# Kernel tuning notes

Measured on AMD Instinct MI355X. Metric: run time of the kernel, lower is better.

## Reference

```python
import jax, jax.numpy as jnp
import numpy as np

B, S, D = 8, 4096, 512
H, DH = 8, 64  # heads, dim_head; inner_dim = H*DH = 512
EPS = 1e-6


def setup_inputs() -> dict:
    key = jax.random.key(0)
    ks = jax.random.split(key, 9)
    scale = 1.0 / np.sqrt(D)
    inner = H * DH
    return {
        "x": jax.random.normal(ks[0], (B, S, D), dtype=jnp.float32),
        "Wq": jax.random.normal(ks[1], (D, inner), dtype=jnp.float32) * scale,
        "bq": jax.random.normal(ks[2], (inner,), dtype=jnp.float32) * 0.01,
        "Wk": jax.random.normal(ks[3], (D, inner), dtype=jnp.float32) * scale,
        "bk": jax.random.normal(ks[4], (inner,), dtype=jnp.float32) * 0.01,
        "Wv": jax.random.normal(ks[5], (D, inner), dtype=jnp.float32) * scale,
        "bv": jax.random.normal(ks[6], (inner,), dtype=jnp.float32) * 0.01,
        "Wo": jax.random.normal(ks[7], (inner, D), dtype=jnp.float32) * (1.0 / np.sqrt(inner)),
        "bo": jax.random.normal(ks[8], (D,), dtype=jnp.float32) * 0.01,
    }


def _phi(x):
    # elu(x) + 1, the fast-transformers default feature map
    return jax.nn.elu(x) + 1.0


def reference(x, Wq, bq, Wk, bk, Wv, bv, Wo, bo):
    b, s, _ = x.shape
    q = (x @ Wq + bq).reshape(b, s, H, DH)
    k = (x @ Wk + bk).reshape(b, s, H, DH)
    v = (x @ Wv + bv).reshape(b, s, H, DH)

    Qf = _phi(q)  # [b, s, h, d]
    Kf = _phi(k)  # [b, s, h, d]

    # KV = sum_s Kf_s (outer) v_s  -> [b, h, d, m]
    KV = jnp.einsum('bshd,bshm->bhdm', Kf, v)
    # normalizer: Z = 1 / (Qf . sum_s Kf + eps)  -> [b, s, h]
    Ksum = Kf.sum(axis=1)  # [b, h, d]
    Z = 1.0 / (jnp.einsum('bshd,bhd->bsh', Qf, Ksum) + EPS)
    out = jnp.einsum('bshd,bhdm,bsh->bshm', Qf, KV, Z)  # [b, s, h, m]

    out = out.reshape(b, s, H * DH)
    return out @ Wo + bo  # dropout is identity at inference
```

## Files before the change

kernel.cpp:

```cpp
#include <hip/hip_runtime.h>
#include <hip/hip_fp16.h>


constexpr int Ss = 4096;
constexpr int Dd = 512;
constexpr int Hh = 8;
constexpr int Mtot = 8 * 4096;
constexpr float EPSF = 1e-6f;

typedef short v8s __attribute__((ext_vector_type(8)));
typedef float v4f __attribute__((ext_vector_type(4)));

__device__ __forceinline__ short f2bf(float f) {
  unsigned u = __float_as_uint(f);
  u += 0x7fff + ((u >> 16) & 1);
  return (short)(u >> 16);
}
__device__ __forceinline__ float bf2f(short s) {
  return __uint_as_float(((unsigned)(unsigned short)s) << 16);
}
__device__ __forceinline__ void async_cp16(const void* g, void* l) {
  __builtin_amdgcn_global_load_lds((__attribute__((address_space(1))) void*)g,
                                   (__attribute__((address_space(3))) void*)l, 16, 0, 0);
}

__global__ __launch_bounds__(256) void prep_w(
    const float* __restrict__ W0, const float* __restrict__ W1,
    const float* __restrict__ W2, const float* __restrict__ W3,
    short* __restrict__ Th, short* __restrict__ Tl)
{
  const float* W = (blockIdx.z == 0) ? W0 : (blockIdx.z == 1) ? W1
                  : (blockIdx.z == 2) ? W2 : W3;
  short* th = Th + (size_t)blockIdx.z * 512 * 512;
  short* tl = Tl + (size_t)blockIdx.z * 512 * 512;
  __shared__ float tile[32][33];
  const int t = threadIdx.x;
  const int tx = t & 31, ty = t >> 5;
  const int k0 = blockIdx.x * 32, n0 = blockIdx.y * 32;
#pragma unroll
  for (int r = 0; r < 32; r += 8)
    tile[ty + r][tx] = W[(size_t)(k0 + ty + r) * 512 + n0 + tx];
  __syncthreads();
#pragma unroll
  for (int r = 0; r < 32; r += 8) {
    const float v = tile[tx][ty + r];
    const short h = f2bf(v);
    const short l = f2bf(v - bf2f(h));
    th[(size_t)(n0 + ty + r) * 512 + k0 + tx] = h;
    tl[(size_t)(n0 + ty + r) * 512 + k0 + tx] = l;
  }
}

__global__ __launch_bounds__(256) void split_x(
    const float* __restrict__ X, short* __restrict__ H, short* __restrict__ L, int n4)
{
  const int i = blockIdx.x * 256 + threadIdx.x;
  if (i >= n4) return;
  const float4 x = reinterpret_cast<const float4*>(X)[i];
  short4 h, l;
  h.x = f2bf(x.x); l.x = f2bf(x.x - bf2f(h.x));
  h.y = f2bf(x.y); l.y = f2bf(x.y - bf2f(h.y));
  h.z = f2bf(x.z); l.z = f2bf(x.z - bf2f(h.z));
  h.w = f2bf(x.w); l.w = f2bf(x.w - bf2f(h.w));
  reinterpret_cast<short4*>(H)[i] = h;
  reinterpret_cast<short4*>(L)[i] = l;
}

__global__ __launch_bounds__(256) void gemm_qkv(
    const short* __restrict__ Ah, const short* __restrict__ Al,
    const short* __restrict__ Wth, const short* __restrict__ Wtl,
    const float* __restrict__ bq, const float* __restrict__ bk,
    const float* __restrict__ bv,
    __half* __restrict__ Qf, __half* __restrict__ Kf, __half* __restrict__ Vv)
{
  constexpr int K = 512;
  __shared__ short As_h[128 * 32], As_l[128 * 32], Bs_h[128 * 32], Bs_l[128 * 32];

  const int mat = blockIdx.y >> 2;
  const int col0 = (blockIdx.y & 3) * 128;
  const int row0 = blockIdx.x * 128;
  const short* Bh = Wth + (size_t)mat * K * 512;
  const short* Bl = Wtl + (size_t)mat * K * 512;
  const float* bias = (mat == 0) ? bq : (mat == 1) ? bk : bv;
  __half* Co = (mat == 0) ? Qf : (mat == 1) ? Kf : Vv;
  const int act = (mat < 2);

  const int t = threadIdx.x;
  const int lane = t & 63;
  const int wv = t >> 6;
  const int wm = wv & 1, wn = wv >> 1;
  const int mr = lane & 15, kq = lane >> 4;

  v4f acc[4][4];
#pragma unroll
  for (int i = 0; i < 4; ++i)
#pragma unroll
    for (int j = 0; j < 4; ++j) acc[i][j] = (v4f){0.f, 0.f, 0.f, 0.f};

  const int srow = t >> 2;
  const int spq = t & 3;

  for (int k0 = 0; k0 < K; k0 += 32) {
#pragma unroll
    for (int c = 0; c < 2; ++c) {
      const int m = c * 64 + srow;
      const int q = spq ^ ((m >> 1) & 3);
      const size_t ga = (size_t)(row0 + m) * K + k0 + q * 8;
      const size_t gb = (size_t)(col0 + m) * K + k0 + q * 8;
      const int lo = c * 2048 + wv * 512;
      async_cp16(Ah + ga, As_h + lo);
      async_cp16(Al + ga, As_l + lo);
      async_cp16(Bh + gb, Bs_h + lo);
      async_cp16(Bl + gb, Bs_l + lo);
    }
    __syncthreads();

    v8s fah[4], fal[4], fbh[4], fbl[4];
#pragma unroll
    for (int i = 0; i < 4; ++i) {
      const int ma = wm * 64 + i * 16 + mr;
      const int pa = kq ^ ((ma >> 1) & 3);
      fah[i] = *reinterpret_cast<const v8s*>(&As_h[ma * 32 + pa * 8]);
      fal[i] = *reinterpret_cast<const v8s*>(&As_l[ma * 32 + pa * 8]);
      const int nb = wn * 64 + i * 16 + mr;
      const int pb = kq ^ ((nb >> 1) & 3);
      fbh[i] = *reinterpret_cast<const v8s*>(&Bs_h[nb * 32 + pb * 8]);
      fbl[i] = *reinterpret_cast<const v8s*>(&Bs_l[nb * 32 + pb * 8]);
    }
#pragma unroll
    for (int i = 0; i < 4; ++i)
#pragma unroll
      for (int j = 0; j < 4; ++j) {
        acc[i][j] = __builtin_amdgcn_mfma_f32_16x16x32_bf16(fah[i], fbh[j], acc[i][j], 0, 0, 0);
        acc[i][j] = __builtin_amdgcn_mfma_f32_16x16x32_bf16(fah[i], fbl[j], acc[i][j], 0, 0, 0);
        acc[i][j] = __builtin_amdgcn_mfma_f32_16x16x32_bf16(fal[i], fbh[j], acc[i][j], 0, 0, 0);
      }
    __syncthreads();
  }

#pragma unroll
  for (int j = 0; j < 4; ++j) {
    const int nc = col0 + wn * 64 + j * 16 + mr;
    const float bz = bias[nc];
#pragma unroll
    for (int i = 0; i < 4; ++i) {
      const int mbase = row0 + wm * 64 + i * 16 + kq * 4;
#pragma unroll
      for (int r = 0; r < 4; ++r) {
        float v = acc[i][j][r] + bz;
        if (act) v = (v > 0.f) ? (v + 1.f) : __expf(v);
        Co[(size_t)(mbase + r) * 512 + nc] = __float2half(v);
      }
    }
  }
}

__global__ __launch_bounds__(256) void gemm_split(
    const short* __restrict__ Ah, const short* __restrict__ Al,
    const short* __restrict__ Bh, const short* __restrict__ Bl,
    const float* __restrict__ bias, float* __restrict__ Cf)
{
  constexpr int K = 512;
  __shared__ short As_h[128 * 32], As_l[128 * 32], Bs_h[128 * 32], Bs_l[128 * 32];
  const int t = threadIdx.x;
  const int lane = t & 63;
  const int wv = t >> 6;
  const int wm = wv & 1, wn = wv >> 1;
  const int row0 = blockIdx.x * 128, col0 = blockIdx.y * 128;
  const int mr = lane & 15, kq = lane >> 4;

  v4f acc[4][4];
#pragma unroll
  for (int i = 0; i < 4; ++i)
#pragma unroll
    for (int j = 0; j < 4; ++j) acc[i][j] = (v4f){0.f, 0.f, 0.f, 0.f};

  const int srow = t >> 2;
  const int spq = t & 3;

  for (int k0 = 0; k0 < K; k0 += 32) {
#pragma unroll
    for (int c = 0; c < 2; ++c) {
      const int m = c * 64 + srow;
      const int q = spq ^ ((m >> 1) & 3);
      const size_t ga = (size_t)(row0 + m) * K + k0 + q * 8;
      const size_t gb = (size_t)(col0 + m) * K + k0 + q * 8;
      const int lo = c * 2048 + wv * 512;
      async_cp16(Ah + ga, As_h + lo);
      async_cp16(Al + ga, As_l + lo);
      async_cp16(Bh + gb, Bs_h + lo);
      async_cp16(Bl + gb, Bs_l + lo);
    }
    __syncthreads();

    v8s fah[4], fal[4], fbh[4], fbl[4];
#pragma unroll
    for (int i = 0; i < 4; ++i) {
      const int ma = wm * 64 + i * 16 + mr;
      const int pa = kq ^ ((ma >> 1) & 3);
      fah[i] = *reinterpret_cast<const v8s*>(&As_h[ma * 32 + pa * 8]);
      fal[i] = *reinterpret_cast<const v8s*>(&As_l[ma * 32 + pa * 8]);
      const int nb = wn * 64 + i * 16 + mr;
      const int pb = kq ^ ((nb >> 1) & 3);
      fbh[i] = *reinterpret_cast<const v8s*>(&Bs_h[nb * 32 + pb * 8]);
      fbl[i] = *reinterpret_cast<const v8s*>(&Bs_l[nb * 32 + pb * 8]);
    }
#pragma unroll
    for (int i = 0; i < 4; ++i)
#pragma unroll
      for (int j = 0; j < 4; ++j) {
        acc[i][j] = __builtin_amdgcn_mfma_f32_16x16x32_bf16(fah[i], fbh[j], acc[i][j], 0, 0, 0);
        acc[i][j] = __builtin_amdgcn_mfma_f32_16x16x32_bf16(fah[i], fbl[j], acc[i][j], 0, 0, 0);
        acc[i][j] = __builtin_amdgcn_mfma_f32_16x16x32_bf16(fal[i], fbh[j], acc[i][j], 0, 0, 0);
      }
    __syncthreads();
  }

#pragma unroll
  for (int j = 0; j < 4; ++j) {
    const int nc = col0 + wn * 64 + j * 16 + mr;
    const float bz = bias[nc];
#pragma unroll
    for (int i = 0; i < 4; ++i) {
      const int mbase = row0 + wm * 64 + i * 16 + kq * 4;
#pragma unroll
      for (int r = 0; r < 4; ++r) Cf[(size_t)(mbase + r) * 512 + nc] = acc[i][j][r] + bz;
    }
  }
}

__global__ __launch_bounds__(256) void kv_stage1(
    const __half* __restrict__ Kf, const __half* __restrict__ V,
    float* __restrict__ KVp, float* __restrict__ Ksp)
{
  const int sc = blockIdx.x, bh = blockIdx.y;
  const int b = bh >> 3, h = bh & 7;
  __shared__ float Ks[64][68];
  __shared__ float Vs[64][68];
  const int tid = threadIdx.x;
  const int dx = (tid >> 4) * 4;
  const int mx = (tid & 15) * 4;
  float acc[4][4];
#pragma unroll
  for (int i = 0; i < 4; ++i)
#pragma unroll
    for (int j = 0; j < 4; ++j) acc[i][j] = 0.f;
  float ksum_acc = 0.f;
  const size_t base = (size_t)b * Ss * Dd + (size_t)h * 64;

  for (int s0 = sc * 256; s0 < sc * 256 + 256; s0 += 64) {
#pragma unroll
    for (int l = 0; l < 2; ++l) {
      const int idx = tid + l * 256;
      const int rr = idx >> 3, cq = idx & 7;
      const size_t g = base + (size_t)(s0 + rr) * Dd + cq * 8;
      const __half2* k2 = reinterpret_cast<const __half2*>(Kf + g);
      const __half2* v2 = reinterpret_cast<const __half2*>(V + g);
#pragma unroll
      for (int u = 0; u < 4; ++u) {
        const float2 kf = __half22float2(k2[u]);
        const float2 vf = __half22float2(v2[u]);
        Ks[rr][cq * 8 + u * 2] = kf.x; Ks[rr][cq * 8 + u * 2 + 1] = kf.y;
        Vs[rr][cq * 8 + u * 2] = vf.x; Vs[rr][cq * 8 + u * 2 + 1] = vf.y;
      }
    }
    __syncthreads();
#pragma unroll 4
    for (int s = 0; s < 64; ++s) {
      const float4 kd = *reinterpret_cast<const float4*>(&Ks[s][dx]);
      const float4 vm = *reinterpret_cast<const float4*>(&Vs[s][mx]);
      const float ka[4] = {kd.x, kd.y, kd.z, kd.w};
      const float va[4] = {vm.x, vm.y, vm.z, vm.w};
#pragma unroll
      for (int i = 0; i < 4; ++i)
#pragma unroll
        for (int j = 0; j < 4; ++j) acc[i][j] = fmaf(ka[i], va[j], acc[i][j]);
    }
    if (tid < 64) {
#pragma unroll 8
      for (int s = 0; s < 64; ++s) ksum_acc += Ks[s][tid];
    }
    __syncthreads();
  }

  const size_t pb = (size_t)(sc * 64 + bh);
#pragma unroll
  for (int i = 0; i < 4; ++i) {
    const float4 ov = {acc[i][0], acc[i][1], acc[i][2], acc[i][3]};
    *reinterpret_cast<float4*>(&KVp[(pb * 64 + dx + i) * 64 + mx]) = ov;
  }
  if (tid < 64) Ksp[pb * 64 + tid] = ksum_acc;
}

__global__ __launch_bounds__(256) void kv_stage2(
    const float* __restrict__ KVp, const float* __restrict__ Ksp,
    float* __restrict__ KV, float* __restrict__ Ksum)
{
  const int bh = blockIdx.x, t = threadIdx.x;
  for (int e = t; e < 4096; e += 256) {
    float s = 0.f;
#pragma unroll
    for (int sc = 0; sc < 16; ++sc) s += KVp[((size_t)(sc * 64 + bh) << 12) + e];
    KV[(size_t)bh * 4096 + e] = s;
  }
  if (t < 64) {
    float s = 0.f;
#pragma unroll
    for (int sc = 0; sc < 16; ++sc) s += Ksp[(size_t)(sc * 64 + bh) * 64 + t];
    Ksum[bh * 64 + t] = s;
  }
}

__global__ __launch_bounds__(256) void attn_combine(
    const __half* __restrict__ Qf, const float* __restrict__ KV,
    const float* __restrict__ Ksum, short* __restrict__ Oh, short* __restrict__ Ol)
{
  const int h = blockIdx.y;
  const int r0 = blockIdx.x * 64;
  const int b = r0 >> 12;
  const int bh = b * Hh + h;
  __shared__ float Qs[64][68];
  __shared__ float KVs[64][68];
  __shared__ float Ksums[64];
  __shared__ float Zs[64];
  const int tid = threadIdx.x;

#pragma unroll
  for (int l = 0; l < 2; ++l) {
    const int idx = tid + l * 256;
    const int rr = idx >> 3, cq = idx & 7;
    const __half2* q2 = reinterpret_cast<const __half2*>(
        Qf + (size_t)(r0 + rr) * Dd + h * 64 + cq * 8);
#pragma unroll
    for (int u = 0; u < 4; ++u) {
      const float2 qf = __half22float2(q2[u]);
      Qs[rr][cq * 8 + u * 2] = qf.x; Qs[rr][cq * 8 + u * 2 + 1] = qf.y;
    }
  }
#pragma unroll
  for (int l = 0; l < 4; ++l) {
    const int idx = tid + l * 256;
    const int rr = idx >> 4, cq = idx & 15;
    *reinterpret_cast<float4*>(&KVs[rr][cq * 4]) = *reinterpret_cast<const float4*>(
        &KV[(size_t)bh * 4096 + rr * 64 + cq * 4]);
  }
  if (tid < 64) Ksums[tid] = Ksum[bh * 64 + tid];
  __syncthreads();

  if (tid < 64) {
    float z = 0.f;
#pragma unroll 8
    for (int d = 0; d < 64; ++d) z = fmaf(Qs[tid][d], Ksums[d], z);
    Zs[tid] = 1.f / (z + EPSF);
  }
  __syncthreads();

  const int rx = (tid >> 4) * 4, mx = (tid & 15) * 4;
  float acc[4][4];
#pragma unroll
  for (int i = 0; i < 4; ++i)
#pragma unroll
    for (int j = 0; j < 4; ++j) acc[i][j] = 0.f;

#pragma unroll 4
  for (int d = 0; d < 64; ++d) {
    const float4 vm = *reinterpret_cast<const float4*>(&KVs[d][mx]);
    const float va[4] = {vm.x, vm.y, vm.z, vm.w};
#pragma unroll
    for (int i = 0; i < 4; ++i) {
      const float q = Qs[rx + i][d];
#pragma unroll
      for (int j = 0; j < 4; ++j) acc[i][j] = fmaf(q, va[j], acc[i][j]);
    }
  }

#pragma unroll
  for (int i = 0; i < 4; ++i) {
    const float z = Zs[rx + i];
    short4 hv, lv;
    float o;
    o = acc[i][0] * z; hv.x = f2bf(o); lv.x = f2bf(o - bf2f(hv.x));
    o = acc[i][1] * z; hv.y = f2bf(o); lv.y = f2bf(o - bf2f(hv.y));
    o = acc[i][2] * z; hv.z = f2bf(o); lv.z = f2bf(o - bf2f(hv.z));
    o = acc[i][3] * z; hv.w = f2bf(o); lv.w = f2bf(o - bf2f(hv.w));
    const size_t off = (size_t)(r0 + rx + i) * Dd + h * 64 + mx;
    *reinterpret_cast<short4*>(&Oh[off]) = hv;
    *reinterpret_cast<short4*>(&Ol[off]) = lv;
  }
}

extern "C" void kernel_launch(void* const* d_in, const int* in_sizes, int n_in,
                              void* d_out, int out_size, void* d_ws, size_t ws_size,
                              hipStream_t stream) {
  const float* x  = (const float*)d_in[0];
  const float* Wq = (const float*)d_in[1];
  const float* bq = (const float*)d_in[2];
  const float* Wk = (const float*)d_in[3];
  const float* bk = (const float*)d_in[4];
  const float* Wv = (const float*)d_in[5];
  const float* bv = (const float*)d_in[6];
  const float* Wo = (const float*)d_in[7];
  const float* bo = (const float*)d_in[8];
  float* out = (float*)d_out;

  char* ws = (char*)d_ws;
  const size_t MB = (size_t)1 << 20;
  short*  x_hi  = (short*)(ws);
  short*  x_lo  = (short*)(ws + 32 * MB);
  short*  Wt_hi = (short*)(ws + 64 * MB);
  short*  Wt_lo = (short*)(ws + 66 * MB);
  __half* Qf    = (__half*)(ws + 68 * MB);
  __half* Kf    = (__half*)(ws + 100 * MB);
  __half* Vv    = (__half*)(ws + 132 * MB);
  float*  KVp   = (float*)(ws + 164 * MB);
  float*  Ksp   = (float*)(ws + 181 * MB);
  float*  KV    = (float*)(ws + 182 * MB);
  float*  Ksum  = (float*)(ws + 183 * MB);
  short*  attn_hi = x_hi;
  short*  attn_lo = x_lo;
  const size_t WSTEP = (size_t)512 * 512;

  prep_w<<<dim3(16, 16, 4), 256, 0, stream>>>(Wq, Wk, Wv, Wo, Wt_hi, Wt_lo);
  split_x<<<Mtot * Dd / 4 / 256, 256, 0, stream>>>(x, x_hi, x_lo, Mtot * Dd / 4);

  gemm_qkv<<<dim3(Mtot / 128, 12), 256, 0, stream>>>(
      x_hi, x_lo, Wt_hi, Wt_lo, bq, bk, bv, Qf, Kf, Vv);

  kv_stage1<<<dim3(16, 64), 256, 0, stream>>>(Kf, Vv, KVp, Ksp);
  kv_stage2<<<64, 256, 0, stream>>>(KVp, Ksp, KV, Ksum);
  attn_combine<<<dim3(Mtot / 64, Hh), 256, 0, stream>>>(Qf, KV, Ksum, attn_hi, attn_lo);

  gemm_split<<<dim3(Mtot / 128, 4), 256, 0, stream>>>(
      attn_hi, attn_lo, Wt_hi + 3 * WSTEP, Wt_lo + 3 * WSTEP, bo, out);
}
```

Measured before the change: 432.9 us.

## Stage GEMM epilogues through swizzled LDS for coalesced stores; halve attn_combine tile

Both GEMM epilogues now write their accumulators into reused shared memory with an XOR swizzle, then write global memory as full 16-byte row-contiguous vectors. The old epilogues issued scattered 2-byte and 4-byte stores. The output GEMM stages its fp32 tile in two column halves so it fits in the existing LDS. attn_combine now processes 32 rows per block instead of 64, which doubles the grid and shrinks per-thread work. The cost is extra barriers and LDS traffic, and each attn_combine block reloads the same KV matrix, so there is more redundant KV loading.

Measured after the change: 473.9 us. 1.09x slower.

```diff
diff --git a/kernel.cpp b/kernel.cpp
--- a/kernel.cpp
+++ b/kernel.cpp
@@ -74,7 +74,11 @@
     __half* __restrict__ Qf, __half* __restrict__ Kf, __half* __restrict__ Vv)
 {
   constexpr int K = 512;
-  __shared__ short As_h[128 * 32], As_l[128 * 32], Bs_h[128 * 32], Bs_l[128 * 32];
+  __shared__ __align__(16) short smem[16384];
+  short* As_h = smem;
+  short* As_l = smem + 4096;
+  short* Bs_h = smem + 8192;
+  short* Bs_l = smem + 12288;
 
   const int mat = blockIdx.y >> 2;
   const int col0 = (blockIdx.y & 3) * 128;
@@ -138,35 +142,54 @@
     __syncthreads();
   }
 
+  __half* hc = reinterpret_cast<__half*>(smem);
 #pragma unroll
   for (int j = 0; j < 4; ++j) {
-    const int nc = col0 + wn * 64 + j * 16 + mr;
-    const float bz = bias[nc];
+    const float bz = bias[col0 + wn * 64 + j * 16 + mr];
 #pragma unroll
     for (int i = 0; i < 4; ++i) {
-      const int mbase = row0 + wm * 64 + i * 16 + kq * 4;
+      const int lr = wm * 64 + i * 16 + kq * 4;
+      const int lc = wn * 64 + (((j * 16) ^ (kq << 4)) + mr);
 #pragma unroll
       for (int r = 0; r < 4; ++r) {
         float v = acc[i][j][r] + bz;
         if (act) v = (v > 0.f) ? (v + 1.f) : __expf(v);
-        Co[(size_t)(mbase + r) * 512 + nc] = __float2half(v);
+        hc[(lr + r) * 128 + lc] = __float2half(v);
       }
     }
   }
-}
-
-__global__ __launch_bounds__(256) void gemm_split(
+  __syncthreads();
+  {
+    const int r = t >> 1, half = (t & 1) * 64;
+    const int sw = ((r >> 2) & 3) << 4;
+    __half* gout = Co + (size_t)(row0 + r) * 512 + col0 + half;
+#pragma unroll
+    for (int u = 0; u < 8; ++u) {
+      const int pc = half + ((u * 8) ^ sw);
+      *reinterpret_cast<v8s*>(gout + u * 8) =
+          *reinterpret_cast<const v8s*>(&hc[r * 128 + pc]);
+    }
+  }
+}
+
+__global__ __launch_bounds__(256) void gemm_out(
     const short* __restrict__ Ah, const short* __restrict__ Al,
     const short* __restrict__ Bh, const short* __restrict__ Bl,
     const float* __restrict__ bias, float* __restrict__ Cf)
 {
   constexpr int K = 512;
-  __shared__ short As_h[128 * 32], As_l[128 * 32], Bs_h[128 * 32], Bs_l[128 * 32];
+  __shared__ __align__(16) short smem[16384];
+  short* As_h = smem;
+  short* As_l = smem + 4096;
+  short* Bs_h = smem + 8192;
+  short* Bs_l = smem + 12288;
+
+  const int col0 = blockIdx.y * 128;
+  const int row0 = blockIdx.x * 128;
   const int t = threadIdx.x;
   const int lane = t & 63;
   const int wv = t >> 6;
   const int wm = wv & 1, wn = wv >> 1;
-  const int row0 = blockIdx.x * 128, col0 = blockIdx.y * 128;
   const int mr = lane & 15, kq = lane >> 4;
 
   v4f acc[4][4];
@@ -216,15 +239,32 @@
     __syncthreads();
   }
 
-#pragma unroll
-  for (int j = 0; j < 4; ++j) {
-    const int nc = col0 + wn * 64 + j * 16 + mr;
-    const float bz = bias[nc];
-#pragma unroll
-    for (int i = 0; i < 4; ++i) {
-      const int mbase = row0 + wm * 64 + i * 16 + kq * 4;
-#pragma unroll
-      for (int r = 0; r < 4; ++r) Cf[(size_t)(mbase + r) * 512 + nc] = acc[i][j][r] + bz;
+  float* fc = reinterpret_cast<float*>(smem);
+#pragma unroll
+  for (int nh = 0; nh < 2; ++nh) {
+    if (nh) __syncthreads();
+    if (wn == nh) {
+#pragma unroll
+      for (int j = 0; j < 4; ++j) {
+        const float bz = bias[col0 + nh * 64 + j * 16 + mr];
+#pragma unroll
+        for (int i = 0; i < 4; ++i) {
+          const int lr = wm * 64 + i * 16 + kq * 4;
+          const int lc = ((j * 16) ^ (kq << 4)) + mr;
+#pragma unroll
+          for (int r = 0; r < 4; ++r) fc[(lr + r) * 64 + lc] = acc[i][j][r] + bz;
+        }
+      }
+    }
+    __syncthreads();
+    const int r = t >> 1, half = (t & 1) * 32;
+    const int sw = ((r >> 2) & 3) << 4;
+    float* gout = Cf + (size_t)(row0 + r) * 512 + col0 + nh * 64 + half;
+#pragma unroll
+    for (int u = 0; u < 8; ++u) {
+      const int pc = (half + u * 4) ^ sw;
+      *reinterpret_cast<float4*>(gout + u * 4) =
+          *reinterpret_cast<const float4*>(&fc[r * 64 + pc]);
     }
   }
 }
@@ -316,19 +356,17 @@
     const float* __restrict__ Ksum, short* __restrict__ Oh, short* __restrict__ Ol)
 {
   const int h = blockIdx.y;
-  const int r0 = blockIdx.x * 64;
+  const int r0 = blockIdx.x * 32;
   const int b = r0 >> 12;
   const int bh = b * Hh + h;
-  __shared__ float Qs[64][68];
+  __shared__ float Qs[32][68];
   __shared__ float KVs[64][68];
   __shared__ float Ksums[64];
-  __shared__ float Zs[64];
+  __shared__ float Zs[32];
   const int tid = threadIdx.x;
 
-#pragma unroll
-  for (int l = 0; l < 2; ++l) {
-    const int idx = tid + l * 256;
-    const int rr = idx >> 3, cq = idx & 7;
+  {
+    const int rr = tid >> 3, cq = tid & 7;
     const __half2* q2 = reinterpret_cast<const __half2*>(
         Qf + (size_t)(r0 + rr) * Dd + h * 64 + cq * 8);
 #pragma unroll
@@ -347,7 +385,7 @@
   if (tid < 64) Ksums[tid] = Ksum[bh * 64 + tid];
   __syncthreads();
 
-  if (tid < 64) {
+  if (tid < 32) {
     float z = 0.f;
 #pragma unroll 8
     for (int d = 0; d < 64; ++d) z = fmaf(Qs[tid][d], Ksums[d], z);
@@ -355,10 +393,10 @@
   }
   __syncthreads();
 
-  const int rx = (tid >> 4) * 4, mx = (tid & 15) * 4;
-  float acc[4][4];
-#pragma unroll
-  for (int i = 0; i < 4; ++i)
+  const int rx = (tid >> 4) * 2, mx = (tid & 15) * 4;
+  float acc[2][4];
+#pragma unroll
+  for (int i = 0; i < 2; ++i)
 #pragma unroll
     for (int j = 0; j < 4; ++j) acc[i][j] = 0.f;
 
@@ -367,7 +405,7 @@
     const float4 vm = *reinterpret_cast<const float4*>(&KVs[d][mx]);
     const float va[4] = {vm.x, vm.y, vm.z, vm.w};
 #pragma unroll
-    for (int i = 0; i < 4; ++i) {
+    for (int i = 0; i < 2; ++i) {
       const float q = Qs[rx + i][d];
 #pragma unroll
       for (int j = 0; j < 4; ++j) acc[i][j] = fmaf(q, va[j], acc[i][j]);
@@ -375,7 +413,7 @@
   }
 
 #pragma unroll
-  for (int i = 0; i < 4; ++i) {
+  for (int i = 0; i < 2; ++i) {
     const float z = Zs[rx + i];
     short4 hv, lv;
     float o;
@@ -428,8 +466,8 @@
 
   kv_stage1<<<dim3(16, 64), 256, 0, stream>>>(Kf, Vv, KVp, Ksp);
   kv_stage2<<<64, 256, 0, stream>>>(KVp, Ksp, KV, Ksum);
-  attn_combine<<<dim3(Mtot / 64, Hh), 256, 0, stream>>>(Qf, KV, Ksum, attn_hi, attn_lo);
-
-  gemm_split<<<dim3(Mtot / 128, 4), 256, 0, stream>>>(
+  attn_combine<<<dim3(Mtot / 32, Hh), 256, 0, stream>>>(Qf, KV, Ksum, attn_hi, attn_lo);
+
+  gemm_out<<<dim3(Mtot / 128, 4), 256, 0, stream>>>(
       attn_hi, attn_lo, Wt_hi + 3 * WSTEP, Wt_lo + 3 * WSTEP, bo, out);
 }
```
